# Optimization experiments

Hardware: AMD Instinct MI355X
Metric: run time of the kernel (lower is better)

## Reference

```python
import jax, jax.numpy as jnp
import numpy as np

B, C, H, W = 4, 64, 160, 160
OUT = 64
KS = (5, 7)


def conv2d(x, w, b=None, pad=0, groups=1):
    y = jax.lax.conv_general_dilated(
        x, w, (1, 1), [(pad, pad), (pad, pad)],
        feature_group_count=groups,
        dimension_numbers=('NCHW', 'OIHW', 'NCHW'))
    return y if b is None else y + b[None, :, None, None]


def bn_eval(x, g, b, m, v, eps=1e-5):
    s = g / jnp.sqrt(v + eps)
    return x * s[None, :, None, None] + (b - m * s)[None, :, None, None]


def boundary_attn(x, w1, b1, w2, b2):
    Cc = x.shape[1]
    kx = jnp.array([[-1., 0., 1.], [-2., 0., 2.], [-1., 0., 1.]], jnp.float32)
    ky = jnp.array([[-1., -2., -1.], [0., 0., 0.], [1., 2., 1.]], jnp.float32)
    sobel = jnp.concatenate([jnp.tile(kx[None, None], (Cc, 1, 1, 1)),
                             jnp.tile(ky[None, None], (Cc, 1, 1, 1))], axis=0)  # [2C,1,3,3]
    # grouped conv (groups=C): same output-channel grouping semantics as torch
    edge = jnp.abs(conv2d(x, sobel, pad=1, groups=Cc))
    edge = (edge[:, :Cc] + edge[:, Cc:]).mean(axis=1, keepdims=True)
    a = jax.nn.relu(conv2d(x, w1, b1, pad=1))
    a = conv2d(a, w2, b2, pad=0)
    a = jax.nn.sigmoid(a + edge)
    return x * a + x


def icc(off, half_k):
    # iterative cumulative constraint over the (small, static) K channel axis
    K = off.shape[1]
    cs = [None] * K
    cs[half_k] = off[:, half_k]
    for i in range(1, half_k + 1):
        cs[half_k - i] = 0.5 * cs[half_k - i + 1] + 0.5 * off[:, half_k - i]
        cs[half_k + i] = 0.5 * cs[half_k + i - 1] + 0.5 * off[:, half_k + i]
    c = jnp.stack(cs, axis=1)
    w = jnp.ones((K, 1, 3, 3), jnp.float32) / 9.0
    return conv2d(c, w, pad=1, groups=K)


def tumor_center(x):
    _, _, Hx, Wx = x.shape
    fs = x.mean(axis=1)  # [B,H,W]
    hg = jnp.arange(Hx, dtype=x.dtype)[None, :, None]
    wg = jnp.arange(Wx, dtype=x.dtype)[None, None, :]
    tot = fs.sum(axis=(1, 2)) + 1e-6
    return (fs * hg).sum(axis=(1, 2)) / tot, (fs * wg).sum(axis=(1, 2)) / tot


def dyn1d(x, kw, kb, K, O):
    # Original Dynamic1DConv reshapes x to [B*H*W, C, 1, 1] and grid_samples a
    # [1,K] grid per pixel. With align_corners=True a 1x1 input maps every grid
    # coordinate to ix=iy=0, so sampled[n,c,k] == x[b,c,h,w] for all k; the
    # bmm with per-pixel kernels followed by sum over C therefore collapses to
    # (sum_c x) * (sum_k kernels) -- same math, no giant gather materialized.
    Bx, _, Hx, Wx = x.shape
    ker = conv2d(x, kw, kb, pad=0).reshape(Bx, O, K, Hx, Wx)
    return x.sum(axis=1, keepdims=True) * ker.sum(axis=2)


def reference(x, ba_w1, ba_b1, ba_w2, ba_b2,
              off_w1, off_b1, off_bn_g, off_bn_b, off_bn_m, off_bn_v,
              off_w2, off_b2,
              rk5_w, rk5_b, rk7_w, rk7_b,
              lk5_w, lk5_b, lk7_w, lk7_b,
              sf_w, sf_b, sf_bn_g, sf_bn_b, sf_bn_m, sf_bn_v,
              fc_w, fc_b):
    residual = x  # in_channels == out_channels -> nn.Identity
    xa = boundary_attn(x, ba_w1, ba_b1, ba_w2, ba_b2)
    # offset branch (faithful to original; mathematically dead because the
    # per-pixel grid_sample ignores its grid -- see dyn1d). BN in eval mode.
    raw = conv2d(xa, off_w1, off_b1, pad=1)
    raw = jax.nn.relu(bn_eval(raw, off_bn_g, off_bn_b, off_bn_m, off_bn_v))
    raw = conv2d(raw, off_w2, off_b2, pad=1)
    sumk, idx = sum(KS), 0
    _offs = []
    for k in KS:
        _offs.append(icc(jnp.tanh(raw[:, idx:idx + k]), k // 2))
        _offs.append(icc(jnp.tanh(raw[:, sumk + idx:sumk + idx + k]), k // 2))
        idx += k
    _hc, _wc = tumor_center(xa)  # also dead w.r.t. output
    O = OUT // 2 // len(KS)  # 16 channels per scale per flow type
    feats = [dyn1d(xa, rk5_w, rk5_b, 5, O), dyn1d(xa, rk7_w, rk7_b, 7, O),
             dyn1d(xa, lk5_w, lk5_b, 5, O), dyn1d(xa, lk7_w, lk7_b, 7, O)]
    fusion = jnp.concatenate(feats, axis=1)  # [B, OUT, H, W]
    y = jax.nn.relu(bn_eval(conv2d(fusion, sf_w, sf_b, pad=1),
                            sf_bn_g, sf_bn_b, sf_bn_m, sf_bn_v))
    y = conv2d(y, fc_w, fc_b, pad=0)
    return y + residual


def setup_inputs() -> dict:
    key = jax.random.key(0)
    keys = iter(jax.random.split(key, 40))
    def nrm(shape, s=0.05):
        return jax.random.normal(next(keys), shape, jnp.float32) * s
    d = {}
    d['x'] = nrm((B, C, H, W), 1.0)
    d['ba_w1'] = nrm((C // 2, C, 3, 3)); d['ba_b1'] = nrm((C // 2,))
    d['ba_w2'] = nrm((1, C // 2, 1, 1)); d['ba_b2'] = nrm((1,))
    d['off_w1'] = nrm((C // 2, C, 3, 3)); d['off_b1'] = nrm((C // 2,))
    d['off_bn_g'] = 1.0 + nrm((C // 2,)); d['off_bn_b'] = nrm((C // 2,))
    d['off_bn_m'] = nrm((C // 2,))
    d['off_bn_v'] = jax.random.uniform(next(keys), (C // 2,), jnp.float32, 0.5, 1.5)
    d['off_w2'] = nrm((2 * sum(KS), C // 2, 3, 3)); d['off_b2'] = nrm((2 * sum(KS),))
    O = OUT // 2 // len(KS)
    for name, k in (('rk5', 5), ('rk7', 7), ('lk5', 5), ('lk7', 7)):
        d[name + '_w'] = nrm((O * k, C, 1, 1)); d[name + '_b'] = nrm((O * k,))
    d['sf_w'] = nrm((OUT, OUT, 3, 3)); d['sf_b'] = nrm((OUT,))
    d['sf_bn_g'] = 1.0 + nrm((OUT,)); d['sf_bn_b'] = nrm((OUT,))
    d['sf_bn_m'] = nrm((OUT,))
    d['sf_bn_v'] = jax.random.uniform(next(keys), (OUT,), jnp.float32, 0.5, 1.5)
    d['fc_w'] = nrm((OUT, OUT, 1, 1)); d['fc_b'] = nrm((OUT,))
    return d
```

## Files before the change

kernel.cpp:

```cpp
#include <hip/hip_runtime.h>
#include <hip/hip_bf16.h>
#include <math.h>

#define BB 4
#define CC 64
#define HH 160
#define WW 160
#define HWs (HH*WW)
#define NPIX (BB*HWs)

using bf16 = __hip_bfloat16;
typedef __attribute__((ext_vector_type(8)))  short short8v;
typedef __attribute__((ext_vector_type(16))) float float16v;

__device__ __forceinline__ unsigned short f2bfu(float f){
    union { bf16 h; unsigned short u; } cv; cv.h = __float2bfloat16(f); return cv.u;
}
__device__ __forceinline__ float bfu2f(unsigned short u){
    union { float f; unsigned int i; } cv; cv.i = ((unsigned int)u)<<16; return cv.f;
}
__device__ __forceinline__ float16v fzero16(){
    float16v z;
    #pragma unroll
    for(int i=0;i<16;i++) z[i]=0.f;
    return z;
}

constexpr int B1X1 = 0;
constexpr int SFBo = 64;
constexpr int SFWf = 128;
constexpr int BAWf = 18560;
constexpr int FUWf = 27776;
constexpr int FCWf = 29824;
constexpr int WS_FLOATS = 31872;

__global__ void k_prep(const float* __restrict__ rk5w, const float* __restrict__ rk5b,
                       const float* __restrict__ rk7w, const float* __restrict__ rk7b,
                       const float* __restrict__ lk5w, const float* __restrict__ lk5b,
                       const float* __restrict__ lk7w, const float* __restrict__ lk7b,
                       const float* __restrict__ sfw,  const float* __restrict__ sfb,
                       const float* __restrict__ bng,  const float* __restrict__ bnb,
                       const float* __restrict__ bnm,  const float* __restrict__ bnv,
                       const float* __restrict__ baw1, const float* __restrict__ fcw,
                       float* __restrict__ ws)
{
    int tid = blockIdx.x*blockDim.x + threadIdx.x;
    int nt  = gridDim.x*blockDim.x;
    for(int o=tid;o<64;o+=nt){
        int grp=o>>4, oo=o&15; int K=(grp&1)?7:5;
        const float* bp = (grp==0)?rk5b:(grp==1)?rk7b:(grp==2)?lk5b:lk7b;
        float s=0.f; for(int k=0;k<K;k++) s += bp[oo*K+k];
        ws[B1X1+o]=s;
    }
    for(int oc=tid;oc<64;oc+=nt){
        float sc = bng[oc]*rsqrtf(bnv[oc]+1e-5f);
        ws[SFBo+oc] = sfb[oc]*sc + bnb[oc] - bnm[oc]*sc;
    }
    unsigned short* sfwf = (unsigned short*)(ws + SFWf);
    for(int idx=tid; idx<36864; idx+=nt){
        int og = idx/18432;  int rem = idx - og*18432;
        int f  = rem>>9;     int r2 = rem & 511;
        int lane = r2>>3;    int j = r2&7;
        int tap = f>>2, kc = f&3;
        int oc = og*32 + (lane&31);
        int ic = kc*16 + (lane>>5)*8 + j;
        float sc = bng[oc]*rsqrtf(bnv[oc]+1e-5f);
        sfwf[idx] = f2bfu(sfw[(oc*64+ic)*9 + tap] * sc);
    }
    unsigned short* bawf = (unsigned short*)(ws + BAWf);
    for(int idx=tid; idx<18432; idx+=nt){
        int f  = idx>>9;     int r2 = idx & 511;
        int lane = r2>>3;    int j = r2&7;
        int tap = f>>2, kc = f&3;
        int oc = lane&31;
        int ic = kc*16 + (lane>>5)*8 + j;
        bawf[idx] = f2bfu(baw1[(oc*64+ic)*9 + tap]);
    }
    unsigned short* fuwf = (unsigned short*)(ws + FUWf);
    for(int idx=tid; idx<4096; idx+=nt){
        int og   = idx>>11;
        int kc   = (idx>>9)&3;
        int lane = (idx>>3)&63;
        int j    = idx&7;
        int oc = og*32 + (lane&31);
        int c  = kc*16 + (lane>>5)*8 + j;
        int grp = oc>>4, oo = oc&15; int K = (grp&1)?7:5;
        const float* w = (grp==0)?rk5w:(grp==1)?rk7w:(grp==2)?lk5w:lk7w;
        float s = 0.f;
        for(int k=0;k<K;k++) s += w[(oo*K+k)*64 + c];
        fuwf[idx] = f2bfu(s);
    }
    unsigned short* fcwf = (unsigned short*)(ws + FCWf);
    for(int idx=tid; idx<4096; idx+=nt){
        int og   = idx>>11;
        int kc   = (idx>>9)&3;
        int lane = (idx>>3)&63;
        int j    = idx&7;
        int oc = og*32 + (lane&31);
        int c  = kc*16 + (lane>>5)*8 + j;
        fcwf[idx] = f2bfu(fcw[oc*64 + c]);
    }
}

__global__ __launch_bounds__(512)
void k_x2nhwc(const float* __restrict__ x, unsigned short* __restrict__ xb)
{
    __shared__ unsigned short ls[256*72];
    const int t = threadIdx.x;
    const int p0 = blockIdx.x*256;
    const int b = p0 / HWs, pp0 = p0 % HWs;
    const float4* xb4 = (const float4*)(x + (size_t)b*CC*HWs + pp0);
    #pragma unroll
    for(int iter=0; iter<4; iter++){
        int item = iter*512 + t;
        int cp = item>>6, g = item&63;
        int c  = cp*2;
        float4 v0 = xb4[(size_t)(c  )*(HWs/4) + g];
        float4 v1 = xb4[(size_t)(c+1)*(HWs/4) + g];
        int px = g*4;
        int bs = (c>>3) ^ ((g>>1)&7);
        float v0a[4] = {v0.x,v0.y,v0.z,v0.w};
        float v1a[4] = {v1.x,v1.y,v1.z,v1.w};
        #pragma unroll
        for(int k=0;k<4;k++){
            unsigned int pk = (unsigned int)f2bfu(v0a[k])
                            | ((unsigned int)f2bfu(v1a[k])<<16);
            *(unsigned int*)(ls + (px+k)*72 + bs*8 + (c&7)) = pk;
        }
    }
    __syncthreads();
    #pragma unroll
    for(int iter=0; iter<4; iter++){
        int idx = iter*512 + t;
        int sub = idx&7, px = idx>>3;
        int bs = sub ^ ((px>>3)&7);
        short8v v = *(short8v*)(ls + px*72 + bs*8);
        *(short8v*)(xb + ((size_t)(p0+px))*64 + sub*8) = v;
    }
}

__global__ __launch_bounds__(512, 4)
void k_fuse(const unsigned short* __restrict__ xb, const float* __restrict__ bab1,
            const float* __restrict__ baw2, const float* __restrict__ bab2,
            const float* __restrict__ ws, const float* __restrict__ fcb,
            const float* __restrict__ x, float* __restrict__ out)
{
    __shared__ unsigned short xt[240*72];
    __shared__ unsigned long long ybex[4*64*2];
    const int bw = blockIdx.x, bh = blockIdx.y, b = blockIdx.z;
    const int t = threadIdx.x;
    const int wave = t>>6, lane = t&63;
    const int half = lane>>5, n = lane&31;
    const int w0 = bw*16, h0 = bh*8;

    const unsigned short* fb = xb + (size_t)b*HWs*64;
    for(int idx=t; idx<1920; idx+=512){
        int sub = idx&7; int pix = idx>>3;
        int r = pix/20, c = pix - r*20;
        int gh = h0-2+r, gw = w0-2+c;
        short8v v = {0,0,0,0,0,0,0,0};
        if(gh>=0&&gh<HH&&gw>=0&&gw<WW)
            v = *(const short8v*)(fb + ((size_t)(gh*WW+gw))*64 + sub*8);
        *(short8v*)(xt + pix*72 + sub*8) = v;
    }
    __syncthreads();

    float cz = 0.f, sx = 0.f;
    if(wave < 6){
        int p = wave*32 + n; if(p > 179) p = 179;
        int pr = p/18, pc = p - pr*18;
        const unsigned short* bawf = (const unsigned short*)(ws + BAWf);
        float16v acc0 = fzero16(), acc1 = fzero16();
        #pragma unroll
        for(int kc=0; kc<4; kc++){
            short8v af[9];
            #pragma unroll
            for(int tap=0; tap<9; tap++)
                af[tap] = *(const short8v*)(bawf + (((size_t)(tap*4+kc))*64 + lane)*8);
            #pragma unroll
            for(int tap=0; tap<9; tap++){
                const int dh = tap/3, dw = tap%3;
                short8v bf = *(const short8v*)(xt + ((pr+dh)*20 + pc+dw)*72
                                               + kc*16 + half*8);
                if(tap&1) acc1 = __builtin_amdgcn_mfma_f32_32x32x16_bf16(af[tap], bf, acc1, 0,0,0);
                else      acc0 = __builtin_amdgcn_mfma_f32_32x32x16_bf16(af[tap], bf, acc0, 0,0,0);
            }
        }
        #pragma unroll
        for(int r=0;r<16;r++){
            int oc = (r&3) + 8*(r>>2) + 4*half;
            cz += fmaxf(acc0[r]+acc1[r]+bab1[oc],0.f)*baw2[oc];
        }
        cz += __shfl_xor(cz, 32);
        short8v ones;
        #pragma unroll
        for(int j=0;j<8;j++) ones[j] = (short)0x3F80;
        float16v s = fzero16();
        #pragma unroll
        for(int kc=0; kc<4; kc++){
            short8v bf = *(const short8v*)(xt + ((pr+1)*20 + pc+1)*72 + kc*16 + half*8);
            s = __builtin_amdgcn_mfma_f32_32x32x16_bf16(ones, bf, s, 0,0,0);
        }
        sx = s[0];
    }
    {
        const int i2 = 511 - t;
        if(i2 < 360){
            const int hf = (i2>=180) ? 1 : 0;
            const int px2 = i2 - hf*180;
            const int r = px2/18, c = px2 - (px2/18)*18;
            float e = 0.f;
            #pragma unroll
            for(int s=0; s<4; s++){
                const int sub = hf*4 + s;
                if(hf==0){
                    short8v a0 = *(const short8v*)(xt + ((r  )*20 + c  )*72 + sub*8);
                    short8v a2 = *(const short8v*)(xt + ((r  )*20 + c+2)*72 + sub*8);
                    short8v a3 = *(const short8v*)(xt + ((r+1)*20 + c  )*72 + sub*8);
                    short8v a5 = *(const short8v*)(xt + ((r+1)*20 + c+2)*72 + sub*8);
                    short8v a6 = *(const short8v*)(xt + ((r+2)*20 + c  )*72 + sub*8);
                    short8v a8 = *(const short8v*)(xt + ((r+2)*20 + c+2)*72 + sub*8);
                    #pragma unroll
                    for(int j=0;j<8;j++){
                        float gx = (bfu2f((unsigned short)a2[j]) - bfu2f((unsigned short)a0[j]))
                           + 2.f*(bfu2f((unsigned short)a5[j]) - bfu2f((unsigned short)a3[j]))
                           +      (bfu2f((unsigned short)a8[j]) - bfu2f((unsigned short)a6[j]));
                        e += fabsf(gx);
                    }
                } else {
                    short8v b0 = *(const short8v*)(xt + ((r  )*20 + c  )*72 + sub*8);
                    short8v b1 = *(const short8v*)(xt + ((r  )*20 + c+1)*72 + sub*8);
                    short8v b2 = *(const short8v*)(xt + ((r  )*20 + c+2)*72 + sub*8);
                    short8v b6 = *(const short8v*)(xt + ((r+2)*20 + c  )*72 + sub*8);
                    short8v b7 = *(const short8v*)(xt + ((r+2)*20 + c+1)*72 + sub*8);
                    short8v b8 = *(const short8v*)(xt + ((r+2)*20 + c+2)*72 + sub*8);
                    #pragma unroll
                    for(int j=0;j<8;j++){
                        float gy = (bfu2f((unsigned short)b6[j]) - bfu2f((unsigned short)b0[j]))
                           + 2.f*(bfu2f((unsigned short)b7[j]) - bfu2f((unsigned short)b1[j]))
                           +      (bfu2f((unsigned short)b8[j]) - bfu2f((unsigned short)b2[j]));
                        e += fabsf(gy);
                    }
                }
            }
            float* ep = (float*)(xt + px2*72 + 64);
            ep[hf] = e;
        }
    }
    __syncthreads();

    if(wave < 6){
        const unsigned short* fuwf = (const unsigned short*)(ws + FUWf);
        int p0g = wave*32 + n;
        bool wr = (p0g < 180);
        int p = wr ? p0g : 179;
        int pr = p/18, pc = p - pr*18;
        const float* ep = (const float*)(xt + p*72 + 64);
        float z = cz + bab2[0] + (ep[0] + ep[1]) * (1.f/32.f);
        float A = 1.f + 1.f/(1.f+__expf(-z));
        float Q = A * sx;
        float P = A * Q;
        unsigned long long pk8[8];
        #pragma unroll
        for(int og=0; og<2; og++){
            float16v a = fzero16();
            #pragma unroll
            for(int kc=0; kc<4; kc++){
                short8v wf = *(const short8v*)(fuwf + (((size_t)og*4 + kc)*64 + lane)*8);
                short8v bf = *(const short8v*)(xt + ((pr+1)*20 + pc+1)*72 + kc*16 + half*8);
                a = __builtin_amdgcn_mfma_f32_32x32x16_bf16(wf, bf, a, 0,0,0);
            }
            float bq[16];
            #pragma unroll
            for(int r=0;r<16;r++) bq[r] = ws[B1X1 + og*32 + (r&3)+8*(r>>2)+4*half];
            #pragma unroll
            for(int gq=0; gq<4; gq++){
                union { unsigned long long u; unsigned short s[4]; } pk;
                #pragma unroll
                for(int rr=0; rr<4; rr++)
                    pk.s[rr] = f2bfu(P*a[4*gq+rr] + Q*bq[4*gq+rr]);
                pk8[og*4+gq] = pk.u;
            }
        }
        if(wr){
            unsigned short* cen = xt + ((pr+1)*20 + pc+1)*72;
            #pragma unroll
            for(int og=0; og<2; og++){
                unsigned short* b2 = cen + og*32 + 4*half;
                #pragma unroll
                for(int gq=0; gq<4; gq++)
                    *(unsigned long long*)(b2 + 8*gq) = pk8[og*4+gq];
            }
        }
    }
    __syncthreads();

    const int rp  = wave & 3;
    const int og  = wave >> 2;
    const int row = 2*rp + (n>>4), col = n&15;
    const unsigned short* sfwf = (const unsigned short*)(ws + SFWf);
    const unsigned short* fcwf = (const unsigned short*)(ws + FCWf);

    float16v Y0 = fzero16(), Y1 = fzero16();
    #pragma unroll
    for(int kc=0; kc<4; kc++){
        short8v af[9];
        #pragma unroll
        for(int tap=0; tap<9; tap++)
            af[tap] = *(const short8v*)(sfwf + (((size_t)og*36 + tap*4+kc)*64 + lane)*8);
        #pragma unroll
        for(int tap=0; tap<9; tap++){
            const int dh = tap/3, dw = tap%3;
            short8v bf = *(const short8v*)(xt + ((row+dh+1)*20 + (col+dw+1))*72
                                           + kc*16 + half*8);
            if(tap&1) Y1 = __builtin_amdgcn_mfma_f32_32x32x16_bf16(af[tap], bf, Y1, 0,0,0);
            else      Y0 = __builtin_amdgcn_mfma_f32_32x32x16_bf16(af[tap], bf, Y0, 0,0,0);
        }
    }
    unsigned short yb[16];
    #pragma unroll
    for(int r=0;r<16;r++){
        float bias = ws[SFBo + og*32 + (r&3)+8*(r>>2)+4*half];
        yb[r] = f2bfu(fmaxf(Y0[r] + Y1[r] + bias, 0.f));
    }
    if(og==1){
        #pragma unroll
        for(int q=0;q<2;q++){
            union { unsigned long long u; unsigned short s[4]; } pk;
            #pragma unroll
            for(int rr=0;rr<4;rr++) pk.s[rr] = yb[4*q+rr];
            ybex[((size_t)rp*64 + lane)*2 + q] = pk.u;
        }
    }
    __syncthreads();
    float16v F0 = fzero16(), F1 = fzero16();
    if(og==0){
        #pragma unroll
        for(int kcl=0; kcl<2; kcl++){
            unsigned short l0,l1,l2,l3, s0,s1,s2,s3;
            if(half==0){ l0=yb[8*kcl+0]; l1=yb[8*kcl+1]; l2=yb[8*kcl+2]; l3=yb[8*kcl+3];
                         s0=yb[8*kcl+4]; s1=yb[8*kcl+5]; s2=yb[8*kcl+6]; s3=yb[8*kcl+7]; }
            else       { l0=yb[8*kcl+4]; l1=yb[8*kcl+5]; l2=yb[8*kcl+6]; l3=yb[8*kcl+7];
                         s0=yb[8*kcl+0]; s1=yb[8*kcl+1]; s2=yb[8*kcl+2]; s3=yb[8*kcl+3]; }
            int p0 = (int)((unsigned)s0 | ((unsigned)s1<<16));
            int p1 = (int)((unsigned)s2 | ((unsigned)s3<<16));
            int r0 = __shfl_xor(p0, 32);
            int r1 = __shfl_xor(p1, 32);
            unsigned short m0 = (unsigned short)(r0 & 0xffff);
            unsigned short m1 = (unsigned short)(((unsigned)r0) >> 16);
            unsigned short m2 = (unsigned short)(r1 & 0xffff);
            unsigned short m3 = (unsigned short)(((unsigned)r1) >> 16);
            short8v B;
            if(half==0){ B[0]=(short)l0; B[1]=(short)l1; B[2]=(short)l2; B[3]=(short)l3;
                         B[4]=(short)m0; B[5]=(short)m1; B[6]=(short)m2; B[7]=(short)m3; }
            else       { B[0]=(short)m0; B[1]=(short)m1; B[2]=(short)m2; B[3]=(short)m3;
                         B[4]=(short)l0; B[5]=(short)l1; B[6]=(short)l2; B[7]=(short)l3; }
            short8v fa0 = *(const short8v*)(fcwf + (((size_t)0*4 + kcl)*64 + lane)*8);
            short8v fa1 = *(const short8v*)(fcwf + (((size_t)1*4 + kcl)*64 + lane)*8);
            F0 = __builtin_amdgcn_mfma_f32_32x32x16_bf16(fa0, B, F0, 0,0,0);
            F1 = __builtin_amdgcn_mfma_f32_32x32x16_bf16(fa1, B, F1, 0,0,0);
        }
        {
            const int srcA  = half ? (lane^32) : lane;
            const int srcB  = half ? lane : (lane^32);
            unsigned long long a03 = ybex[((size_t)rp*64 + srcA)*2 + half];
            unsigned long long a47 = ybex[((size_t)rp*64 + srcB)*2 + half];
            short8v B;
            #pragma unroll
            for(int j2=0;j2<4;j2++){
                B[j2]   = (short)(unsigned short)((a03 >> (16*j2)) & 0xffff);
                B[4+j2] = (short)(unsigned short)((a47 >> (16*j2)) & 0xffff);
            }
            short8v fa0 = *(const short8v*)(fcwf + (((size_t)0*4 + 2)*64 + lane)*8);
            short8v fa1 = *(const short8v*)(fcwf + (((size_t)1*4 + 2)*64 + lane)*8);
            F0 = __builtin_amdgcn_mfma_f32_32x32x16_bf16(fa0, B, F0, 0,0,0);
            F1 = __builtin_amdgcn_mfma_f32_32x32x16_bf16(fa1, B, F1, 0,0,0);
        }
    }
    __syncthreads();
    if(og==1){
        #pragma unroll
        for(int q=0;q<2;q++){
            union { unsigned long long u; unsigned short s[4]; } pk;
            #pragma unroll
            for(int rr=0;rr<4;rr++) pk.s[rr] = yb[4*(q+2)+rr];
            ybex[((size_t)rp*64 + lane)*2 + q] = pk.u;
        }
    }
    __syncthreads();
    if(og==0){
        {
            const int srcA  = half ? (lane^32) : lane;
            const int srcB  = half ? lane : (lane^32);
            unsigned long long a03 = ybex[((size_t)rp*64 + srcA)*2 + half];
            unsigned long long a47 = ybex[((size_t)rp*64 + srcB)*2 + half];
            short8v B;
            #pragma unroll
            for(int j2=0;j2<4;j2++){
                B[j2]   = (short)(unsigned short)((a03 >> (16*j2)) & 0xffff);
                B[4+j2] = (short)(unsigned short)((a47 >> (16*j2)) & 0xffff);
            }
            short8v fa0 = *(const short8v*)(fcwf + (((size_t)0*4 + 3)*64 + lane)*8);
            short8v fa1 = *(const short8v*)(fcwf + (((size_t)1*4 + 3)*64 + lane)*8);
            F0 = __builtin_amdgcn_mfma_f32_32x32x16_bf16(fa0, B, F0, 0,0,0);
            F1 = __builtin_amdgcn_mfma_f32_32x32x16_bf16(fa1, B, F1, 0,0,0);
        }
        #pragma unroll
        for(int og2=0; og2<2; og2++){
            #pragma unroll
            for(int r=0;r<16;r++){
                int oc = og2*32 + (r&3)+8*(r>>2)+4*half;
                size_t g = ((size_t)(b*CC + oc))*HWs + (h0+row)*WW + w0 + col;
                float v = (og2==0) ? F0[r] : F1[r];
                out[g] = v + fcb[oc] + x[g];
            }
        }
    }
}

extern "C" void kernel_launch(void* const* d_in, const int* in_sizes, int n_in,
                              void* d_out, int out_size, void* d_ws, size_t ws_size,
                              hipStream_t stream)
{
    const float* x     = (const float*)d_in[0];
    const float* ba_w1 = (const float*)d_in[1];
    const float* ba_b1 = (const float*)d_in[2];
    const float* ba_w2 = (const float*)d_in[3];
    const float* ba_b2 = (const float*)d_in[4];
    const float* rk5_w = (const float*)d_in[13];
    const float* rk5_b = (const float*)d_in[14];
    const float* rk7_w = (const float*)d_in[15];
    const float* rk7_b = (const float*)d_in[16];
    const float* lk5_w = (const float*)d_in[17];
    const float* lk5_b = (const float*)d_in[18];
    const float* lk7_w = (const float*)d_in[19];
    const float* lk7_b = (const float*)d_in[20];
    const float* sf_w  = (const float*)d_in[21];
    const float* sf_b  = (const float*)d_in[22];
    const float* bng   = (const float*)d_in[23];
    const float* bnb   = (const float*)d_in[24];
    const float* bnm   = (const float*)d_in[25];
    const float* bnv   = (const float*)d_in[26];
    const float* fc_w  = (const float*)d_in[27];
    const float* fc_b  = (const float*)d_in[28];

    float* wsf = (float*)d_ws;
    unsigned short* XB  = (unsigned short*)((char*)d_ws + (size_t)WS_FLOATS*4);
    float* out = (float*)d_out;

    k_prep<<<64, 256, 0, stream>>>(rk5_w,rk5_b,rk7_w,rk7_b,lk5_w,lk5_b,lk7_w,lk7_b,
                                   sf_w,sf_b,bng,bnb,bnm,bnv, ba_w1, fc_w, wsf);
    k_x2nhwc<<<NPIX/256, 512, 0, stream>>>(x, XB);
    k_fuse<<<dim3(10,20,4), 512, 0, stream>>>(XB, ba_b1, ba_w2, ba_b2, wsf, fc_b, x, out);
}
```

Measured before the change: 177.7 us.

## Fuse NCHW-to-NHWC bf16 conversion into main kernel halo tile load

Removes the separate transpose kernel that wrote a bf16 NHWC copy of the input. The fused kernel now reads fp32 NCHW directly as float4 rows per channel pair, converts to bf16 and writes the channel-interleaved tile with halo into shared memory. This saves one launch and a full write-plus-read of the intermediate. In exchange, each tile re-reads its halo in fp32 (twice the bytes per element), and the shared-memory writes are strided 4-byte stores that may hit bank conflicts.

```diff
diff --git a/kernel.cpp b/kernel.cpp
--- a/kernel.cpp
+++ b/kernel.cpp
@@ -102,48 +102,11 @@
     }
 }
 
-__global__ __launch_bounds__(512)
-void k_x2nhwc(const float* __restrict__ x, unsigned short* __restrict__ xb)
-{
-    __shared__ unsigned short ls[256*72];
-    const int t = threadIdx.x;
-    const int p0 = blockIdx.x*256;
-    const int b = p0 / HWs, pp0 = p0 % HWs;
-    const float4* xb4 = (const float4*)(x + (size_t)b*CC*HWs + pp0);
-    #pragma unroll
-    for(int iter=0; iter<4; iter++){
-        int item = iter*512 + t;
-        int cp = item>>6, g = item&63;
-        int c  = cp*2;
-        float4 v0 = xb4[(size_t)(c  )*(HWs/4) + g];
-        float4 v1 = xb4[(size_t)(c+1)*(HWs/4) + g];
-        int px = g*4;
-        int bs = (c>>3) ^ ((g>>1)&7);
-        float v0a[4] = {v0.x,v0.y,v0.z,v0.w};
-        float v1a[4] = {v1.x,v1.y,v1.z,v1.w};
-        #pragma unroll
-        for(int k=0;k<4;k++){
-            unsigned int pk = (unsigned int)f2bfu(v0a[k])
-                            | ((unsigned int)f2bfu(v1a[k])<<16);
-            *(unsigned int*)(ls + (px+k)*72 + bs*8 + (c&7)) = pk;
-        }
-    }
-    __syncthreads();
-    #pragma unroll
-    for(int iter=0; iter<4; iter++){
-        int idx = iter*512 + t;
-        int sub = idx&7, px = idx>>3;
-        int bs = sub ^ ((px>>3)&7);
-        short8v v = *(short8v*)(ls + px*72 + bs*8);
-        *(short8v*)(xb + ((size_t)(p0+px))*64 + sub*8) = v;
-    }
-}
-
 __global__ __launch_bounds__(512, 4)
-void k_fuse(const unsigned short* __restrict__ xb, const float* __restrict__ bab1,
+void k_fuse(const float* __restrict__ x, const float* __restrict__ bab1,
             const float* __restrict__ baw2, const float* __restrict__ bab2,
             const float* __restrict__ ws, const float* __restrict__ fcb,
-            const float* __restrict__ x, float* __restrict__ out)
+            float* __restrict__ out)
 {
     __shared__ unsigned short xt[240*72];
     __shared__ unsigned long long ybex[4*64*2];
@@ -153,15 +116,40 @@
     const int half = lane>>5, n = lane&31;
     const int w0 = bw*16, h0 = bh*8;
 
-    const unsigned short* fb = xb + (size_t)b*HWs*64;
-    for(int idx=t; idx<1920; idx+=512){
-        int sub = idx&7; int pix = idx>>3;
-        int r = pix/20, c = pix - r*20;
-        int gh = h0-2+r, gw = w0-2+c;
-        short8v v = {0,0,0,0,0,0,0,0};
-        if(gh>=0&&gh<HH&&gw>=0&&gw<WW)
-            v = *(const short8v*)(fb + ((size_t)(gh*WW+gw))*64 + sub*8);
-        *(short8v*)(xt + pix*72 + sub*8) = v;
+    {
+        const float* xb0 = x + (size_t)b*CC*HWs;
+        #pragma unroll
+        for(int it=0; it<5; it++){
+            int item = it*512 + t;
+            if(item < 2304){
+                int cp  = item/72;
+                int rem = item - cp*72;
+                int r   = rem/6, g = rem - r*6;
+                int c   = cp*2;
+                int gh  = h0-2+r;
+                int gwb = w0-4+g*4;
+                bool rowok = ((unsigned)gh  < (unsigned)HH);
+                bool colok = ((unsigned)gwb <= (unsigned)(WW-4));
+                bool ok = rowok && colok;
+                int ghc  = rowok ? gh  : 0;
+                int gwbc = colok ? gwb : 0;
+                const float4 v0 = *(const float4*)(xb0 + (size_t)(c  )*HWs + ghc*WW + gwbc);
+                const float4 v1 = *(const float4*)(xb0 + (size_t)(c+1)*HWs + ghc*WW + gwbc);
+                float v0a[4] = {v0.x,v0.y,v0.z,v0.w};
+                float v1a[4] = {v1.x,v1.y,v1.z,v1.w};
+                #pragma unroll
+                for(int k=0;k<4;k++){
+                    int cl = g*4 + k - 2;
+                    if((unsigned)cl < 20u){
+                        float a0 = ok ? v0a[k] : 0.f;
+                        float a1 = ok ? v1a[k] : 0.f;
+                        unsigned int pk = (unsigned int)f2bfu(a0)
+                                        | ((unsigned int)f2bfu(a1)<<16);
+                        *(unsigned int*)(xt + (r*20+cl)*72 + c) = pk;
+                    }
+                }
+            }
+        }
     }
     __syncthreads();
 
@@ -445,11 +433,9 @@
     const float* fc_b  = (const float*)d_in[28];
 
     float* wsf = (float*)d_ws;
-    unsigned short* XB  = (unsigned short*)((char*)d_ws + (size_t)WS_FLOATS*4);
     float* out = (float*)d_out;
 
     k_prep<<<64, 256, 0, stream>>>(rk5_w,rk5_b,rk7_w,rk7_b,lk5_w,lk5_b,lk7_w,lk7_b,
                                    sf_w,sf_b,bng,bnb,bnm,bnv, ba_w1, fc_w, wsf);
-    k_x2nhwc<<<NPIX/256, 512, 0, stream>>>(x, XB);
-    k_fuse<<<dim3(10,20,4), 512, 0, stream>>>(XB, ba_b1, ba_w2, ba_b2, wsf, fc_b, x, out);
-}
+    k_fuse<<<dim3(10,20,4), 512, 0, stream>>>(x, ba_b1, ba_w2, ba_b2, wsf, fc_b, out);
+}
```

After: 178.8 us. Within noise of the previous version (+0.6%).
